# Optimization experiments

Hardware: AMD Instinct MI355X
Metric: run time of the kernel (lower is better)

Reference implementation:

```python
import jax, jax.numpy as jnp
import numpy as np

ALPHA = 0.9
CAND_LEN_LIMIT = 16
DOC_LEN_LIMIT = 256
EMBED_DIM = 768
BATCH = 8


def _tri_num(n):
    return n * (n + 1) // 2


def _build_alpha_buffers(doc_len, max_cand_len, alpha):
    """Vectorized construction of the 5 FOFE context alpha buffers.

    Candidate c = (start i, span s) enumerated by start then span, matching the
    original get_contexts_alpha_buffers ordering. end e = i + s.
      buf0 candidate ctx      : alpha^(e-j) for i <= j <= e
      buf1 left ctx excl cand : alpha^(i-1-j) for j <= i-1 (zero when i == 0)
      buf2 left ctx incl cand : alpha^(e-j) for j <= e
      buf3 right ctx excl cand: alpha^(j-1-e) for j >= e+1
      buf4 right ctx incl cand: alpha^(j-i) for j >= i
    """
    starts, spans = [], []
    for i in range(doc_len):
        n = max_cand_len if i < doc_len - max_cand_len else doc_len - i
        starts += [i] * n
        spans += list(range(n))
    s = np.asarray(starts)[:, None]              # [n_cand, 1]
    e = (np.asarray(starts) + np.asarray(spans))[:, None]
    j = np.arange(doc_len)[None, :]              # [1, doc_len]

    def pw(p, m):
        return np.where(m, alpha ** np.where(m, p, 0), 0.0).astype(np.float32)

    buf0 = pw(e - j, (j >= s) & (j <= e))
    buf1 = pw(s - 1 - j, (j <= s - 1) & (s > 0))
    buf2 = pw(e - j, j <= e)
    buf3 = pw(j - 1 - e, j >= e + 1)
    buf4 = pw(j - s, j >= s)
    cands_pos = np.concatenate([s, e], axis=1).astype(np.float32)  # [n_cand, 2]
    return (buf0, buf1, buf2, buf3, buf4), cands_pos


def setup_inputs() -> dict:
    key = jax.random.key(0)
    k1, k2 = jax.random.split(key)
    x_input = jax.random.normal(k1, (BATCH, DOC_LEN_LIMIT, EMBED_DIM), dtype=jnp.float32)
    x_mask = jax.random.randint(k2, (BATCH, DOC_LEN_LIMIT), 0, 2, dtype=jnp.int32)
    return {"x_input": x_input, "x_mask": x_mask}


def reference(x_input, x_mask):
    batch = x_input.shape[0]
    doc_len = min(x_input.shape[1], DOC_LEN_LIMIT)
    max_cand_len = min(CAND_LEN_LIMIT, doc_len)
    bufs_np, cands_pos_np = _build_alpha_buffers(doc_len, max_cand_len, ALPHA)
    buf0, buf1, buf2, buf3, buf4 = [jnp.asarray(b) for b in bufs_np]
    n_cand = buf0.shape[0]

    # concat order for has_lr_ctx_cand_incl and has_lr_ctx_cand_excl both True:
    # [left_excl, left_incl, cand, right_incl, right_excl]
    all_bufs = jnp.stack([buf1, buf2, buf0, buf4, buf3], axis=0)  # [5, n_cand, L]
    # one big contraction instead of 5 bmms
    codes = jnp.einsum('kcl,bld->bkcd', all_bufs, x_input)        # [B,5,n_cand,D]
    fofe_codes = codes.transpose(0, 2, 1, 3).reshape(batch, n_cand, 5 * x_input.shape[2])

    cands_pos = jnp.broadcast_to(jnp.asarray(cands_pos_np)[None], (batch, n_cand, 2))
    padded_cands = (jnp.einsum('cl,bl->bc', buf0, x_mask.astype(jnp.float32))[..., None] > 0)
    return fofe_codes, cands_pos, padded_cands
```

## Files before the change

### kernel.cpp

```cpp
#include <hip/hip_runtime.h>

#define NB 8
#define LEN 256
#define DIM 768
#define NC 3976
#define OFF_POS 122142720
#define OFF_PAD (122142720 + 63616)

constexpr float ALPHA_F = 0.9f;
constexpr float A32 = 0.03433683820292512f;

typedef float f4 __attribute__((ext_vector_type(4)));

__global__ __launch_bounds__(256) void scan_kernel(const float* __restrict__ x,
                                                   float* __restrict__ P,
                                                   float* __restrict__ S) {
    const int dl = threadIdx.x & 31;
    const int chunk = threadIdx.x >> 5;
    const int d = blockIdx.x * 32 + dl;
    const int b = blockIdx.y;
    const int dir = blockIdx.z;
    const float* __restrict__ xb = x + (size_t)b * LEN * DIM;
    float* __restrict__ ob = (dir ? S : P) + (size_t)b * LEN * DIM;

    float vals[32];
    float acc = 0.f;
#pragma unroll
    for (int t = 0; t < 32; ++t) {
        const int lm = chunk * 32 + t;
        const int l = dir ? (LEN - 1 - lm) : lm;
        acc = fmaf(ALPHA_F, acc, xb[l * DIM + d]);
        vals[t] = acc;
    }

    __shared__ float ends[8][32];
    ends[chunk][dl] = acc;
    __syncthreads();

    float carry = 0.f;
    for (int k = 0; k < chunk; ++k)
        carry = fmaf(A32, carry, ends[k][dl]);

    float w = ALPHA_F;
#pragma unroll
    for (int t = 0; t < 32; ++t) {
        const int lm = chunk * 32 + t;
        const int l = dir ? (LEN - 1 - lm) : lm;
        ob[l * DIM + d] = fmaf(w, carry, vals[t]);
        w *= ALPHA_F;
    }
}

__global__ __launch_bounds__(192) void out_kernel(const float* __restrict__ P,
                                                  const float* __restrict__ S,
                                                  const int* __restrict__ mask,
                                                  float* __restrict__ out) {
    const int b = blockIdx.x;
    const int i = blockIdx.y;
    const int t = threadIdx.x;

    int n, c0;
    if (i <= 240) {
        n = 16;
        c0 = i * 16;
    } else {
        const int r = LEN - i;
        n = r;
        c0 = 3856 + 120 - r * (r + 1) / 2;
    }

    const f4 z4 = (f4)0.f;
    const f4* __restrict__ Pb = (const f4*)(P + (size_t)b * LEN * DIM);
    const f4* __restrict__ Sb = (const f4*)(S + (size_t)b * LEN * DIM);

    const f4 pm1 = (i > 0) ? Pb[(i - 1) * 192 + t] : z4;
    const f4 si = Sb[i * 192 + t];

    f4* o = (f4*)out + (size_t)(b * NC + c0) * 960 + t;
    float w = ALPHA_F;
    for (int s = 0; s < n; ++s) {
        const int e = i + s;
        const f4 pe = Pb[e * 192 + t];
        const f4 se1 = (e < LEN - 1) ? Sb[(e + 1) * 192 + t] : z4;
        const f4 cand = pe - w * pm1;

        __builtin_nontemporal_store(pm1, o + 0 * 192);
        __builtin_nontemporal_store(pe, o + 1 * 192);
        __builtin_nontemporal_store(cand, o + 2 * 192);
        __builtin_nontemporal_store(si, o + 3 * 192);
        __builtin_nontemporal_store(se1, o + 4 * 192);
        o += 960;
        w *= ALPHA_F;
    }

    if (t < 64) {
        const int m = (t < n) ? mask[b * LEN + i + t] : 0;
        const unsigned long long ball = __ballot(m != 0);
        if (t < n) {
            const size_t c = (size_t)(b * NC + c0 + t);
            out[OFF_POS + c * 2] = (float)i;
            out[OFF_POS + c * 2 + 1] = (float)(i + t);
            out[OFF_PAD + c] = (ball & ((2ull << t) - 1)) ? 1.f : 0.f;
        }
    }
}

extern "C" void kernel_launch(void* const* d_in, const int* in_sizes, int n_in,
                              void* d_out, int out_size, void* d_ws, size_t ws_size,
                              hipStream_t stream) {
    const float* x = (const float*)d_in[0];
    const int* mask = (const int*)d_in[1];
    float* out = (float*)d_out;
    float* P = (float*)d_ws;
    float* S = P + (size_t)NB * LEN * DIM;

    scan_kernel<<<dim3(DIM / 32, NB, 2), 256, 0, stream>>>(x, P, S);
    out_kernel<<<dim3(NB, LEN), 192, 0, stream>>>(P, S, mask, out);
}
```

Baseline: 110.3 us.

## Fuse scan into output kernel with truncated per-block recurrence recompute

Drops the separate prefix/suffix scan kernel and its global workspace. Each block of 192 threads now handles G=4 candidate starts and recomputes the FOFE prefix and suffix recurrences in registers. It starts each recurrence KTRUNC=64 positions back, relying on 0.9^64 being small. The aim is to remove the workspace write and re-read and one kernel launch from a store-bound kernel. In exchange, every block does redundant input reads, register pressure rises (arrays of 20 f4 values), and the truncated recurrence adds a small numerical error.

```diff
diff --git a/kernel.cpp b/kernel.cpp
--- a/kernel.cpp
+++ b/kernel.cpp
@@ -6,101 +6,99 @@
 #define NC 3976
 #define OFF_POS 122142720
 #define OFF_PAD (122142720 + 63616)
+#define G 4
+#define KTRUNC 64
 
 constexpr float ALPHA_F = 0.9f;
-constexpr float A32 = 0.03433683820292512f;
 
 typedef float f4 __attribute__((ext_vector_type(4)));
 
-__global__ __launch_bounds__(256) void scan_kernel(const float* __restrict__ x,
-                                                   float* __restrict__ P,
-                                                   float* __restrict__ S) {
-    const int dl = threadIdx.x & 31;
-    const int chunk = threadIdx.x >> 5;
-    const int d = blockIdx.x * 32 + dl;
-    const int b = blockIdx.y;
-    const int dir = blockIdx.z;
-    const float* __restrict__ xb = x + (size_t)b * LEN * DIM;
-    float* __restrict__ ob = (dir ? S : P) + (size_t)b * LEN * DIM;
+__global__ __launch_bounds__(192, 2) void fused_kernel(const float* __restrict__ x,
+                                                       const int* __restrict__ mask,
+                                                       float* __restrict__ out) {
+    const int b = blockIdx.x;
+    const int i0 = blockIdx.y * G;
+    const int t = threadIdx.x;
+    const f4* __restrict__ xb = (const f4*)(x + (size_t)b * LEN * DIM);
 
-    float vals[32];
-    float acc = 0.f;
+    f4 P[G + 16];
+    f4 acc = (f4)0.f;
+    {
+        int l0 = i0 - 1 - KTRUNC;
+        if (l0 < 0) l0 = 0;
+#pragma unroll 8
+        for (int l = l0; l <= i0 - 2; ++l)
+            acc = acc * ALPHA_F + xb[l * 192 + t];
 #pragma unroll
-    for (int t = 0; t < 32; ++t) {
-        const int lm = chunk * 32 + t;
-        const int l = dir ? (LEN - 1 - lm) : lm;
-        acc = fmaf(ALPHA_F, acc, xb[l * DIM + d]);
-        vals[t] = acc;
+        for (int r = 0; r < G + 16; ++r) {
+            const int l = i0 - 1 + r;
+            if (l >= 0 && l < LEN) acc = acc * ALPHA_F + xb[l * 192 + t];
+            P[r] = acc;
+        }
     }
 
-    __shared__ float ends[8][32];
-    ends[chunk][dl] = acc;
-    __syncthreads();
-
-    float carry = 0.f;
-    for (int k = 0; k < chunk; ++k)
-        carry = fmaf(A32, carry, ends[k][dl]);
-
-    float w = ALPHA_F;
+    f4 S[G + 16];
+    acc = (f4)0.f;
+    {
+        int l1 = i0 + G + 15 + KTRUNC;
+        if (l1 > LEN - 1) l1 = LEN - 1;
+#pragma unroll 8
+        for (int l = l1; l > i0 + G + 15; --l)
+            acc = acc * ALPHA_F + xb[l * 192 + t];
 #pragma unroll
-    for (int t = 0; t < 32; ++t) {
-        const int lm = chunk * 32 + t;
-        const int l = dir ? (LEN - 1 - lm) : lm;
-        ob[l * DIM + d] = fmaf(w, carry, vals[t]);
-        w *= ALPHA_F;
-    }
-}
-
-__global__ __launch_bounds__(192) void out_kernel(const float* __restrict__ P,
-                                                  const float* __restrict__ S,
-                                                  const int* __restrict__ mask,
-                                                  float* __restrict__ out) {
-    const int b = blockIdx.x;
-    const int i = blockIdx.y;
-    const int t = threadIdx.x;
-
-    int n, c0;
-    if (i <= 240) {
-        n = 16;
-        c0 = i * 16;
-    } else {
-        const int r = LEN - i;
-        n = r;
-        c0 = 3856 + 120 - r * (r + 1) / 2;
+        for (int r = G + 15; r >= 0; --r) {
+            const int l = i0 + r;
+            if (l < LEN) {
+                acc = acc * ALPHA_F + xb[l * 192 + t];
+                S[r] = acc;
+            } else {
+                S[r] = (f4)0.f;
+            }
+        }
     }
 
-    const f4 z4 = (f4)0.f;
-    const f4* __restrict__ Pb = (const f4*)(P + (size_t)b * LEN * DIM);
-    const f4* __restrict__ Sb = (const f4*)(S + (size_t)b * LEN * DIM);
+#pragma unroll
+    for (int g = 0; g < G; ++g) {
+        const int i = i0 + g;
+        int n, c0;
+        if (i <= LEN - 16) {
+            n = 16;
+            c0 = i * 16;
+        } else {
+            const int r = LEN - i;
+            n = r;
+            c0 = 3856 + 120 - r * (r + 1) / 2;
+        }
+        const f4 pm1 = P[g];
+        const f4 si = S[g];
 
-    const f4 pm1 = (i > 0) ? Pb[(i - 1) * 192 + t] : z4;
-    const f4 si = Sb[i * 192 + t];
+        f4* o = (f4*)out + (size_t)(b * NC + c0) * 960 + t;
+        float w = ALPHA_F;
+#pragma unroll
+        for (int s = 0; s < 16; ++s) {
+            if (s < n) {
+                const f4 pe = P[g + 1 + s];
+                const f4 se1 = S[g + 1 + s];
+                const f4 cand = pe - w * pm1;
+                __builtin_nontemporal_store(pm1, o + 0 * 192);
+                __builtin_nontemporal_store(pe, o + 1 * 192);
+                __builtin_nontemporal_store(cand, o + 2 * 192);
+                __builtin_nontemporal_store(si, o + 3 * 192);
+                __builtin_nontemporal_store(se1, o + 4 * 192);
+                o += 960;
+            }
+            w *= ALPHA_F;
+        }
 
-    f4* o = (f4*)out + (size_t)(b * NC + c0) * 960 + t;
-    float w = ALPHA_F;
-    for (int s = 0; s < n; ++s) {
-        const int e = i + s;
-        const f4 pe = Pb[e * 192 + t];
-        const f4 se1 = (e < LEN - 1) ? Sb[(e + 1) * 192 + t] : z4;
-        const f4 cand = pe - w * pm1;
-
-        __builtin_nontemporal_store(pm1, o + 0 * 192);
-        __builtin_nontemporal_store(pe, o + 1 * 192);
-        __builtin_nontemporal_store(cand, o + 2 * 192);
-        __builtin_nontemporal_store(si, o + 3 * 192);
-        __builtin_nontemporal_store(se1, o + 4 * 192);
-        o += 960;
-        w *= ALPHA_F;
-    }
-
-    if (t < 64) {
-        const int m = (t < n) ? mask[b * LEN + i + t] : 0;
-        const unsigned long long ball = __ballot(m != 0);
-        if (t < n) {
-            const size_t c = (size_t)(b * NC + c0 + t);
-            out[OFF_POS + c * 2] = (float)i;
-            out[OFF_POS + c * 2 + 1] = (float)(i + t);
-            out[OFF_PAD + c] = (ball & ((2ull << t) - 1)) ? 1.f : 0.f;
+        if (t < 64) {
+            const int m = (t < n) ? mask[b * LEN + i + t] : 0;
+            const unsigned long long ball = __ballot(m != 0);
+            if (t < n) {
+                const size_t c = (size_t)(b * NC + c0 + t);
+                out[OFF_POS + c * 2] = (float)i;
+                out[OFF_POS + c * 2 + 1] = (float)(i + t);
+                out[OFF_PAD + c] = (ball & ((2ull << t) - 1)) ? 1.f : 0.f;
+            }
         }
     }
 }
@@ -111,9 +109,5 @@
     const float* x = (const float*)d_in[0];
     const int* mask = (const int*)d_in[1];
     float* out = (float*)d_out;
-    float* P = (float*)d_ws;
-    float* S = P + (size_t)NB * LEN * DIM;
-
-    scan_kernel<<<dim3(DIM / 32, NB, 2), 256, 0, stream>>>(x, P, S);
-    out_kernel<<<dim3(NB, LEN), 192, 0, stream>>>(P, S, mask, out);
+    fused_kernel<<<dim3(NB, LEN / G), 192, 0, stream>>>(x, mask, out);
 }
```

Measured after the change: 108.8 us. Within noise of the previous version (-1.3%).
